# Performance work log

Measured on AMD Instinct MI355X. Metric: run time of the kernel, lower is better.

## Reference

```python
import jax, jax.numpy as jnp
import numpy as np

EPS = 1e-6

def fexp(x, p):
    # signed power used in superquadric parametrization
    return jnp.sign(x) * (jnp.abs(x) + EPS) ** p

def quat_to_rot(q):
    q = q / (jnp.linalg.norm(q, axis=-1, keepdims=True) + EPS)
    w, x, y, z = q[..., 0], q[..., 1], q[..., 2], q[..., 3]
    R = jnp.stack([
        jnp.stack([1 - 2 * (y * y + z * z), 2 * (x * y - w * z), 2 * (x * z + w * y)], -1),
        jnp.stack([2 * (x * y + w * z), 1 - 2 * (x * x + z * z), 2 * (y * z - w * x)], -1),
        jnp.stack([2 * (x * z - w * y), 2 * (y * z + w * x), 1 - 2 * (x * x + y * y)], -1),
    ], -2)
    return R  # (..., 3, 3)

def setup_inputs() -> dict:
    key = jax.random.key(0)
    ks = jax.random.split(key, 9)
    B, M, S, N = 8, 16, 100, 2048
    pcl = jax.random.normal(ks[0], (B, N, 3), jnp.float32)
    translations = 0.5 * jax.random.normal(ks[1], (B, M, 3), jnp.float32)
    rotations = jax.random.normal(ks[2], (B, M, 4), jnp.float32)
    size = 0.2 + 0.6 * jax.random.uniform(ks[3], (B, M, 3), jnp.float32)
    shape_eps = 0.4 + 1.2 * jax.random.uniform(ks[4], (B, M, 2), jnp.float32)
    deformations = 0.6 * jax.random.uniform(ks[5], (B, M, 2), jnp.float32) - 0.3
    probabilities = jax.random.uniform(ks[6], (B, M), jnp.float32, 0.05, 0.95)
    etas = jax.random.uniform(ks[7], (S,), jnp.float32, -np.pi / 2, np.pi / 2)
    omegas = jax.random.uniform(ks[8], (S,), jnp.float32, -np.pi, np.pi)
    return {"pcl": pcl, "translations": translations, "rotations": rotations,
            "size": size, "shape_eps": shape_eps, "deformations": deformations,
            "probabilities": probabilities, "etas": etas, "omegas": omegas}

def reference(pcl, translations, rotations, size, shape_eps, deformations, probabilities, etas, omegas):
    B, N, _ = pcl.shape
    M = translations.shape[1]
    # transform pcl into primitive-centric frames: (B,N,M,3)
    R = quat_to_rot(rotations)                                   # (B,M,3,3)
    d = pcl[:, :, None, :] - translations[:, None, :, :]         # (B,N,M,3)
    pcl_t = jnp.einsum('bmij,bnmj->bnmi', R, d)                  # (B,N,M,3)
    # sample superquadric surfaces: (B,M,S,3)
    e1 = shape_eps[..., 0:1]; e2 = shape_eps[..., 1:2]           # (B,M,1)
    a1 = size[..., 0:1]; a2 = size[..., 1:2]; a3 = size[..., 2:3]
    ce = fexp(jnp.cos(etas)[None, None, :], e1)
    se = fexp(jnp.sin(etas)[None, None, :], e1)
    cw = fexp(jnp.cos(omegas)[None, None, :], e2)
    sw = fexp(jnp.sin(omegas)[None, None, :], e2)
    x = a1 * ce * cw; y = a2 * ce * sw; z = a3 * se              # (B,M,S)
    # tapering deformation
    fx = deformations[..., 0:1] * z / a3 + 1.0
    fy = deformations[..., 1:2] * z / a3 + 1.0
    points = jnp.stack([fx * x, fy * y, z], -1)                  # (B,M,S,3)
    # pairwise squared distances: (B,M,S,N)
    diff = points[:, :, :, None, :] - jnp.transpose(pcl_t, (0, 2, 1, 3))[:, :, None, :, :]
    dist = jnp.sum(diff * diff, -1)
    # --- pcl_to_prim loss ---
    dmin = jnp.transpose(jnp.min(dist, axis=2), (0, 2, 1))       # (B,N,M)
    idx = jnp.argsort(dmin, axis=-1)
    distance = jnp.take_along_axis(dmin, idx, axis=-1)
    probs_g = jax.vmap(lambda p, i: p[i])(probabilities, idx)    # (B,N,M)
    neg_cp = jnp.cumprod(1.0 - probs_g, axis=-1)
    neg_cp = jnp.concatenate([jnp.ones_like(neg_cp[..., :1]), neg_cp[..., :-1]], -1)
    minprob = probs_g * neg_cp
    pcl_to_prim = jnp.sum(distance * minprob) / (B * N)
    # --- prim_to_pcl loss ---
    dminN = jnp.min(dist, axis=3)                                # (B,M,S)
    dminN = jnp.where(dminN >= 1e30, 0.0, dminN)
    s0, s1, s2 = size[..., 0], size[..., 1], size[..., 2]
    area = 4 * np.pi * ((s0 * s1) ** 1.6 / 3 + (s0 * s2) ** 1.6 / 3 + (s1 * s2) ** 1.6 / 3) ** 0.625
    area = M * area / jnp.sum(area, axis=-1, keepdims=True)
    prim_to_pcl = jnp.sum(jnp.mean(dminN, -1) * area) / (B * M)
    # regularizer weights are zero (regularizer_type=None path) -> regs = 0
    return pcl_to_prim + prim_to_pcl
```

## Files before the change

kernel.cpp:

```cpp
#include <hip/hip_runtime.h>
#include <math.h>

#define EPSF 1e-6f

constexpr int B = 8, N = 2048, M = 16, S = 100;
constexpr int MAIN_BLOCKS = B * (N / 64);
constexpr int PRIM_BLOCKS = B * M * 2;
constexpr int TOTAL_BLOCKS = MAIN_BLOCKS + PRIM_BLOCKS;
constexpr int NPART = MAIN_BLOCKS * 4 + PRIM_BLOCKS;

__device__ __forceinline__ float fexp_d(float x, float p) {
    float sg = (x > 0.f) ? 1.f : ((x < 0.f) ? -1.f : 0.f);
    return sg * __powf(fabsf(x) + EPSF, p);
}

__device__ __forceinline__ void quat_R(const float* __restrict__ rot, int bm, float R[9]) {
    float w = rot[bm * 4 + 0], x = rot[bm * 4 + 1], y = rot[bm * 4 + 2], z = rot[bm * 4 + 3];
    float inv = 1.0f / (sqrtf(w * w + x * x + y * y + z * z) + EPSF);
    w *= inv; x *= inv; y *= inv; z *= inv;
    R[0] = 1.f - 2.f * (y * y + z * z); R[1] = 2.f * (x * y - w * z); R[2] = 2.f * (x * z + w * y);
    R[3] = 2.f * (x * y + w * z); R[4] = 1.f - 2.f * (x * x + z * z); R[5] = 2.f * (y * z - w * x);
    R[6] = 2.f * (x * z - w * y); R[7] = 2.f * (y * z + w * x); R[8] = 1.f - 2.f * (x * x + y * y);
}

__device__ __forceinline__ float4 surf_point(
    const float* __restrict__ sizep, const float* __restrict__ seps,
    const float* __restrict__ deform, const float* __restrict__ etas,
    const float* __restrict__ omegas, int bm, int s)
{
    float e1 = seps[bm * 2 + 0], e2 = seps[bm * 2 + 1];
    float a1 = sizep[bm * 3 + 0], a2 = sizep[bm * 3 + 1], a3 = sizep[bm * 3 + 2];
    float d0 = deform[bm * 2 + 0], d1 = deform[bm * 2 + 1];
    float se_, ce_, sw_, cw_;
    __sincosf(etas[s], &se_, &ce_);
    __sincosf(omegas[s], &sw_, &cw_);
    float ce = fexp_d(ce_, e1);
    float se = fexp_d(se_, e1);
    float cw = fexp_d(cw_, e2);
    float sw = fexp_d(sw_, e2);
    float x = a1 * ce * cw;
    float y = a2 * ce * sw;
    float z = a3 * se;
    float fx = d0 * (z / a3) + 1.0f;
    float fy = d1 * (z / a3) + 1.0f;
    float4 P;
    P.x = fx * x; P.y = fy * y; P.z = z;
    P.w = P.x * P.x + P.y * P.y + P.z * P.z;
    return P;
}

__global__ __launch_bounds__(256) void k_all(
    const float* __restrict__ pcl, const float* __restrict__ trans,
    const float* __restrict__ rot, const float* __restrict__ sizep,
    const float* __restrict__ seps, const float* __restrict__ deform,
    const float* __restrict__ probs,
    const float* __restrict__ etas, const float* __restrict__ omegas,
    float* __restrict__ part)
{
    __shared__ float4 pts[S * M];
    __shared__ float sbuf[20];

    int t = threadIdx.x;

    if (blockIdx.x < MAIN_BLOCKS) {
        int b  = blockIdx.x >> 5;
        int n0 = (blockIdx.x & 31) * 64;

        for (int i = t; i < S * M; i += 256) {
            int s = i >> 4, m = i & 15;
            pts[i] = surf_point(sizep, seps, deform, etas, omegas, b * M + m, s);
        }
        __syncthreads();

        int m  = t & 15;
        int nl = t >> 4;
        int bm = b * M + m;
        float R[9];
        quat_R(rot, bm, R);
        float tx = trans[bm * 3 + 0], ty = trans[bm * 3 + 1], tz = trans[bm * 3 + 2];

        float mx[4], my[4], mz[4], psq[4], dmin[4];
#pragma unroll
        for (int j = 0; j < 4; j++) {
            int n = n0 + nl + 16 * j;
            float px = pcl[(b * N + n) * 3 + 0];
            float py = pcl[(b * N + n) * 3 + 1];
            float pz = pcl[(b * N + n) * 3 + 2];
            float dx = px - tx, dy = py - ty, dz = pz - tz;
            float X = R[0] * dx + R[1] * dy + R[2] * dz;
            float Y = R[3] * dx + R[4] * dy + R[5] * dz;
            float Z = R[6] * dx + R[7] * dy + R[8] * dz;
            mx[j] = -2.f * X; my[j] = -2.f * Y; mz[j] = -2.f * Z;
            psq[j] = X * X + Y * Y + Z * Z;
            dmin[j] = 3.4e38f;
        }

        float4 Pa[4], Pb[4];
#pragma unroll
        for (int u = 0; u < 4; u++) Pa[u] = pts[u * M + m];
        for (int s = 0; s < S; s += 4) {
#pragma unroll
            for (int u = 0; u < 4; u++) {
                int sn = s + 4 + u; if (sn >= S) sn = S - 1;
                Pb[u] = pts[sn * M + m];
            }
#pragma unroll
            for (int u = 0; u < 4; u++) {
                float4 P = Pa[u];
#pragma unroll
                for (int j = 0; j < 4; j++) {
                    float d = fmaf(P.x, mx[j], P.w);
                    d = fmaf(P.y, my[j], d);
                    d = fmaf(P.z, mz[j], d);
                    dmin[j] = fminf(dmin[j], d);
                }
            }
#pragma unroll
            for (int u = 0; u < 4; u++) Pa[u] = Pb[u];
        }

        float ompr[16];
#pragma unroll
        for (int k = 0; k < 16; k++) ompr[k] = 1.f - probs[b * M + k];
        float pv  = probs[bm];
        float acc = 0.f;
#pragma unroll
        for (int j = 0; j < 4; j++) {
            float key = dmin[j] + psq[j];
            float prod = 1.f;
#pragma unroll
            for (int k = 0; k < 16; k++) {
                float bk = __shfl(key, k, 16);
                bool before = (bk < key) || (bk == key && k < m);
                prod *= before ? ompr[k] : 1.f;
            }
            acc += key * pv * prod;
        }
        for (int off = 32; off >= 1; off >>= 1) acc += __shfl_down(acc, off);
        if ((t & 63) == 0)
            part[blockIdx.x * 4 + (t >> 6)] = acc * (1.0f / (B * N));
    } else {
        int pb = blockIdx.x - MAIN_BLOCKS;
        int bm = pb >> 1, q = pb & 1;
        int b = bm >> 4, m = bm & 15;
        int s0 = q * 50;

        float4* spts = pts;
        float* sarea = sbuf;
        float* wsum  = sbuf + 16;

        if (t < 50) spts[t] = surf_point(sizep, seps, deform, etas, omegas, bm, s0 + t);
        if (t >= 64 && t < 64 + M) {
            int mm = t - 64;
            float s0s = sizep[(b * M + mm) * 3 + 0];
            float s1s = sizep[(b * M + mm) * 3 + 1];
            float s2s = sizep[(b * M + mm) * 3 + 2];
            float tt = __powf(s0s * s1s, 1.6f) / 3.f + __powf(s0s * s2s, 1.6f) / 3.f
                     + __powf(s1s * s2s, 1.6f) / 3.f;
            sarea[mm] = 4.0f * 3.14159265358979323846f * __powf(tt, 0.625f);
        }
        __syncthreads();

        float R[9];
        quat_R(rot, bm, R);
        float tx = trans[bm * 3 + 0], ty = trans[bm * 3 + 1], tz = trans[bm * 3 + 2];

        int w = t >> 6, lane = t & 63;
        int cnt = (w < 2) ? 13 : 12;
        int off = (w < 2) ? w * 13 : 26 + (w - 2) * 12;

        float px[13], py[13], pz[13], mins[13];
#pragma unroll
        for (int k = 0; k < 13; k++) {
            int sl = (k < cnt) ? (off + k) : off;
            float4 P = spts[sl];
            px[k] = P.x; py[k] = P.y; pz[k] = P.z;
            mins[k] = 3.4e38f;
        }

        const float* pcb = pcl + b * N * 3;
        float cx = pcb[lane * 3 + 0], cy = pcb[lane * 3 + 1], cz = pcb[lane * 3 + 2];
        for (int i = 0; i < 32; i++) {
            int n2 = (i < 31) ? ((i + 1) * 64 + lane) : lane;
            float nx = pcb[n2 * 3 + 0], ny = pcb[n2 * 3 + 1], nz = pcb[n2 * 3 + 2];
            float dx = cx - tx, dy = cy - ty, dz = cz - tz;
            float X = R[0] * dx + R[1] * dy + R[2] * dz;
            float Y = R[3] * dx + R[4] * dy + R[5] * dz;
            float Z = R[6] * dx + R[7] * dy + R[8] * dz;
            float mX = -2.f * X, mY = -2.f * Y, mZ = -2.f * Z;
            float Xsq = X * X + Y * Y + Z * Z;
#pragma unroll
            for (int k = 0; k < 13; k++) {
                float d = fmaf(px[k], mX, Xsq);
                d = fmaf(py[k], mY, d);
                d = fmaf(pz[k], mZ, d);
                mins[k] = fminf(mins[k], d);
            }
            cx = nx; cy = ny; cz = nz;
        }

        float sum = 0.f;
#pragma unroll
        for (int k = 0; k < 13; k++) {
            float v = mins[k];
            for (int o = 32; o >= 1; o >>= 1) v = fminf(v, __shfl_down(v, o));
            int sl = (k < cnt) ? (off + k) : off;
            v += spts[sl].w;
            sum += (k < cnt) ? v : 0.f;
        }

        if (lane == 0) wsum[w] = sum;
        __syncthreads();
        if (t == 0) {
            float total = wsum[0] + wsum[1] + wsum[2] + wsum[3];
            float asum = 0.f;
            for (int mm = 0; mm < M; mm++) asum += sarea[mm];
            float area = (float)M * sarea[m] / asum;
            part[MAIN_BLOCKS * 4 + pb] = total * area * (1.0f / (S * B * M));
        }
    }
}

__global__ __launch_bounds__(256) void k_reduce(const float* __restrict__ part,
                                               float* __restrict__ out)
{
    __shared__ float ws[4];
    int t = threadIdx.x;
    float s = 0.f;
    for (int i = t; i < NPART; i += 256) s += part[i];
    for (int off = 32; off >= 1; off >>= 1) s += __shfl_down(s, off);
    if ((t & 63) == 0) ws[t >> 6] = s;
    __syncthreads();
    if (t == 0) out[0] = ws[0] + ws[1] + ws[2] + ws[3];
}

extern "C" void kernel_launch(void* const* d_in, const int* in_sizes, int n_in,
                              void* d_out, int out_size, void* d_ws, size_t ws_size,
                              hipStream_t stream)
{
    const float* pcl    = (const float*)d_in[0];
    const float* trans  = (const float*)d_in[1];
    const float* rot    = (const float*)d_in[2];
    const float* sizep  = (const float*)d_in[3];
    const float* seps   = (const float*)d_in[4];
    const float* deform = (const float*)d_in[5];
    const float* probs  = (const float*)d_in[6];
    const float* etas   = (const float*)d_in[7];
    const float* omegas = (const float*)d_in[8];
    float* out  = (float*)d_out;
    float* partials = (float*)d_ws;

    k_all<<<TOTAL_BLOCKS, 256, 0, stream>>>(pcl, trans, rot, sizep, seps, deform,
                                            probs, etas, omegas, partials);
    k_reduce<<<1, 256, 0, stream>>>(partials, out);
}
```

Before: 93.10 us.

## Fuse final reduction via completion flags and precompute trig logs in shared memory

Drops the separate reduce kernel launch. One extra block spin-waits on per-block release flags, sums the partials, then resets the flags for the next call. Surface-point generation in the main blocks now precomputes per-sample sincos log2/sign values in shared memory once, so each point needs only exp2 calls instead of full powf and sincos. The flag scheme depends on the waiting block not starving producer blocks and on the workspace flags starting at zero.

```diff
diff --git a/kernel.cpp b/kernel.cpp
--- a/kernel.cpp
+++ b/kernel.cpp
@@ -9,9 +9,16 @@
 constexpr int TOTAL_BLOCKS = MAIN_BLOCKS + PRIM_BLOCKS;
 constexpr int NPART = MAIN_BLOCKS * 4 + PRIM_BLOCKS;
 
+__device__ __forceinline__ float hw_exp2(float x) { return __builtin_amdgcn_exp2f(x); }
+__device__ __forceinline__ float hw_log2(float x) { return __builtin_amdgcn_logf(x); }
+
 __device__ __forceinline__ float fexp_d(float x, float p) {
     float sg = (x > 0.f) ? 1.f : ((x < 0.f) ? -1.f : 0.f);
     return sg * __powf(fabsf(x) + EPSF, p);
+}
+
+__device__ __forceinline__ float sgn_d(float x) {
+    return (x > 0.f) ? 1.f : ((x < 0.f) ? -1.f : 0.f);
 }
 
 __device__ __forceinline__ void quat_R(const float* __restrict__ rot, int bm, float R[9]) {
@@ -55,9 +62,11 @@
     const float* __restrict__ seps, const float* __restrict__ deform,
     const float* __restrict__ probs,
     const float* __restrict__ etas, const float* __restrict__ omegas,
-    float* __restrict__ part)
+    float* __restrict__ part, unsigned int* __restrict__ flags,
+    float* __restrict__ out)
 {
     __shared__ float4 pts[S * M];
+    __shared__ float trig[S * 8];
     __shared__ float sbuf[20];
 
     int t = threadIdx.x;
@@ -66,9 +75,40 @@
         int b  = blockIdx.x >> 5;
         int n0 = (blockIdx.x & 31) * 64;
 
+        if (t < S) {
+            float se_, ce_, sw_, cw_;
+            __sincosf(etas[t], &se_, &ce_);
+            __sincosf(omegas[t], &sw_, &cw_);
+            trig[t * 8 + 0] = hw_log2(fabsf(ce_) + EPSF);
+            trig[t * 8 + 1] = sgn_d(ce_);
+            trig[t * 8 + 2] = hw_log2(fabsf(se_) + EPSF);
+            trig[t * 8 + 3] = sgn_d(se_);
+            trig[t * 8 + 4] = hw_log2(fabsf(cw_) + EPSF);
+            trig[t * 8 + 5] = sgn_d(cw_);
+            trig[t * 8 + 6] = hw_log2(fabsf(sw_) + EPSF);
+            trig[t * 8 + 7] = sgn_d(sw_);
+        }
+        __syncthreads();
+
         for (int i = t; i < S * M; i += 256) {
-            int s = i >> 4, m = i & 15;
-            pts[i] = surf_point(sizep, seps, deform, etas, omegas, b * M + m, s);
+            int s = i >> 4, mm = i & 15;
+            int bmi = b * M + mm;
+            float e1 = seps[bmi * 2 + 0], e2 = seps[bmi * 2 + 1];
+            float a1 = sizep[bmi * 3 + 0], a2 = sizep[bmi * 3 + 1], a3 = sizep[bmi * 3 + 2];
+            float d0 = deform[bmi * 2 + 0], d1 = deform[bmi * 2 + 1];
+            float ce = trig[s * 8 + 1] * hw_exp2(e1 * trig[s * 8 + 0]);
+            float se = trig[s * 8 + 3] * hw_exp2(e1 * trig[s * 8 + 2]);
+            float cw = trig[s * 8 + 5] * hw_exp2(e2 * trig[s * 8 + 4]);
+            float sw = trig[s * 8 + 7] * hw_exp2(e2 * trig[s * 8 + 6]);
+            float x = a1 * ce * cw;
+            float y = a2 * ce * sw;
+            float z = a3 * se;
+            float fx = fmaf(d0, se, 1.0f);
+            float fy = fmaf(d1, se, 1.0f);
+            float4 P;
+            P.x = fx * x; P.y = fy * y; P.z = z;
+            P.w = P.x * P.x + P.y * P.y + P.z * P.z;
+            pts[i] = P;
         }
         __syncthreads();
 
@@ -138,8 +178,14 @@
         }
         for (int off = 32; off >= 1; off >>= 1) acc += __shfl_down(acc, off);
         if ((t & 63) == 0)
-            part[blockIdx.x * 4 + (t >> 6)] = acc * (1.0f / (B * N));
-    } else {
+            __hip_atomic_store(&part[blockIdx.x * 4 + (t >> 6)],
+                               acc * (1.0f / (B * N)),
+                               __ATOMIC_RELAXED, __HIP_MEMORY_SCOPE_AGENT);
+        __syncthreads();
+        if (t == 0)
+            __hip_atomic_store(&flags[blockIdx.x], 1u,
+                               __ATOMIC_RELEASE, __HIP_MEMORY_SCOPE_AGENT);
+    } else if (blockIdx.x < TOTAL_BLOCKS) {
         int pb = blockIdx.x - MAIN_BLOCKS;
         int bm = pb >> 1, q = pb & 1;
         int b = bm >> 4, m = bm & 15;
@@ -216,22 +262,30 @@
             float asum = 0.f;
             for (int mm = 0; mm < M; mm++) asum += sarea[mm];
             float area = (float)M * sarea[m] / asum;
-            part[MAIN_BLOCKS * 4 + pb] = total * area * (1.0f / (S * B * M));
-        }
+            __hip_atomic_store(&part[MAIN_BLOCKS * 4 + pb],
+                               total * area * (1.0f / (S * B * M)),
+                               __ATOMIC_RELAXED, __HIP_MEMORY_SCOPE_AGENT);
+            __hip_atomic_store(&flags[blockIdx.x], 1u,
+                               __ATOMIC_RELEASE, __HIP_MEMORY_SCOPE_AGENT);
+        }
+    } else {
+        if (t >= 64) return;
+        for (int i = t; i < TOTAL_BLOCKS; i += 64) {
+            while (__hip_atomic_load(&flags[i], __ATOMIC_ACQUIRE,
+                                     __HIP_MEMORY_SCOPE_AGENT) != 1u)
+                __builtin_amdgcn_s_sleep(2);
+        }
+        __threadfence();
+        float ssum = 0.f;
+        for (int i = t; i < NPART; i += 64)
+            ssum += __hip_atomic_load(&part[i], __ATOMIC_RELAXED,
+                                      __HIP_MEMORY_SCOPE_AGENT);
+        for (int off = 32; off >= 1; off >>= 1) ssum += __shfl_down(ssum, off);
+        if (t == 0) out[0] = ssum;
+        for (int i = t; i < TOTAL_BLOCKS; i += 64)
+            __hip_atomic_store(&flags[i], 0u, __ATOMIC_RELAXED,
+                               __HIP_MEMORY_SCOPE_AGENT);
     }
-}
-
-__global__ __launch_bounds__(256) void k_reduce(const float* __restrict__ part,
-                                               float* __restrict__ out)
-{
-    __shared__ float ws[4];
-    int t = threadIdx.x;
-    float s = 0.f;
-    for (int i = t; i < NPART; i += 256) s += part[i];
-    for (int off = 32; off >= 1; off >>= 1) s += __shfl_down(s, off);
-    if ((t & 63) == 0) ws[t >> 6] = s;
-    __syncthreads();
-    if (t == 0) out[0] = ws[0] + ws[1] + ws[2] + ws[3];
 }
 
 extern "C" void kernel_launch(void* const* d_in, const int* in_sizes, int n_in,
@@ -247,10 +301,11 @@
     const float* probs  = (const float*)d_in[6];
     const float* etas   = (const float*)d_in[7];
     const float* omegas = (const float*)d_in[8];
-    float* out  = (float*)d_out;
+    float* out = (float*)d_out;
     float* partials = (float*)d_ws;
-
-    k_all<<<TOTAL_BLOCKS, 256, 0, stream>>>(pcl, trans, rot, sizep, seps, deform,
-                                            probs, etas, omegas, partials);
-    k_reduce<<<1, 256, 0, stream>>>(partials, out);
-}
+    unsigned int* flags = (unsigned int*)((char*)d_ws + 8192);
+
+    k_all<<<TOTAL_BLOCKS + 1, 256, 0, stream>>>(pcl, trans, rot, sizep, seps,
+                                                deform, probs, etas, omegas,
+                                                partials, flags, out);
+}
```

New measurement: 91.74 us. No clear change (-1.5%).
